# Kernel optimization log

Measured on AMD Instinct MI355X. Metric: run time of the kernel, lower is better.

## Reference

```python
import jax, jax.numpy as jnp
import numpy as np

INT8_MAX = 127.0

def setup_inputs() -> dict:
    key = jax.random.key(0)
    k1, k2, k3, k4 = jax.random.split(key, 4)
    B, T, IN, OUT = 1, 8192, 4096, 12288
    input_tensor = jax.random.normal(k1, (B, T, IN), dtype=jnp.float32)
    # pre-quantized int8 weight, symmetric range [-127, 127]
    weight = jax.random.randint(k2, (OUT, IN), -127, 128, dtype=jnp.int8)
    # per-output-row weight scales (small positive)
    weight_scale = (jax.random.uniform(k3, (OUT, 1), dtype=jnp.float32) * 0.01 + 1e-4)
    bias = jax.random.normal(k4, (OUT,), dtype=jnp.float32)
    return {"input_tensor": input_tensor, "weight": weight,
            "weight_scale": weight_scale, "bias": bias}

def reference(input_tensor, weight, weight_scale, bias):
    # input_tensor: [1, T, IN] -> squeeze leading dim as in torch forward
    x = input_tensor[0]  # [T, IN]
    # per-token symmetric int8 quantization (scaled_int8_quant, symmetric=True)
    absmax = jnp.max(jnp.abs(x), axis=-1, keepdims=True)            # [T, 1]
    x_scale = jnp.maximum(absmax, 1e-8) / INT8_MAX                  # [T, 1]
    x_q = jnp.clip(jnp.round(x / x_scale), -INT8_MAX, INT8_MAX).astype(jnp.int8)
    # int8 GEMM with int32 accumulation: [T, IN] x [IN, OUT]
    acc = jax.lax.dot_general(x_q, weight.T,
                              (((1,), (0,)), ((), ())),
                              preferred_element_type=jnp.int32)     # [T, OUT]
    # fused dequant epilogue: per-token scale * per-channel scale + bias
    out = acc.astype(jnp.float32) * x_scale * weight_scale[:, 0][None, :] + bias[None, :]
    return out[None]  # [1, T, OUT]
```

## Files before the change

kernel.cpp:

```cpp
#include <hip/hip_runtime.h>
#include <stdint.h>

#define T_TOKENS 8192
#define K_IN 4096
#define N_OUT 12288

using int32x4 = __attribute__((ext_vector_type(4))) int;

__global__ void quant_rows(const float* __restrict__ x,
                           int8_t* __restrict__ xq,
                           float* __restrict__ xs) {
    const int t = blockIdx.x;
    const int tid = threadIdx.x;
    const float* row = x + (size_t)t * K_IN;
    float4 v[4];
    float am = 0.0f;
#pragma unroll
    for (int i = 0; i < 4; ++i) {
        v[i] = ((const float4*)row)[tid + 256 * i];
        am = fmaxf(am, fmaxf(fmaxf(fabsf(v[i].x), fabsf(v[i].y)),
                             fmaxf(fabsf(v[i].z), fabsf(v[i].w))));
    }
#pragma unroll
    for (int off = 32; off > 0; off >>= 1)
        am = fmaxf(am, __shfl_xor(am, off));
    __shared__ float red[4];
    if ((tid & 63) == 0) red[tid >> 6] = am;
    __syncthreads();
    am = fmaxf(fmaxf(red[0], red[1]), fmaxf(red[2], red[3]));
    const float scale = fmaxf(am, 1e-8f) / 127.0f;
    if (tid == 0) xs[t] = scale;
    char4* dst = (char4*)(xq + (size_t)t * K_IN);
#pragma unroll
    for (int i = 0; i < 4; ++i) {
        float4 f = v[i];
        char4 c;
        float r;
        r = fminf(fmaxf(rintf(f.x / scale), -127.0f), 127.0f); c.x = (signed char)(int)r;
        r = fminf(fmaxf(rintf(f.y / scale), -127.0f), 127.0f); c.y = (signed char)(int)r;
        r = fminf(fmaxf(rintf(f.z / scale), -127.0f), 127.0f); c.z = (signed char)(int)r;
        r = fminf(fmaxf(rintf(f.w / scale), -127.0f), 127.0f); c.w = (signed char)(int)r;
        dst[tid + 256 * i] = c;
    }
}

__global__ void pack_weight(const int* __restrict__ w, int8_t* __restrict__ wq) {
    const int idx = blockIdx.x * 256 + threadIdx.x;
    int4 v = ((const int4*)w)[idx];
    char4 c;
    c.x = (signed char)v.x; c.y = (signed char)v.y;
    c.z = (signed char)v.z; c.w = (signed char)v.w;
    ((char4*)wq)[idx] = c;
}

__global__ __launch_bounds__(256) void gemm_i8(
        const int8_t* __restrict__ Aq, const int8_t* __restrict__ Bq,
        const float* __restrict__ xs, const float* __restrict__ wsc,
        const float* __restrict__ bias, float* __restrict__ out) {
    __shared__ __align__(16) int8_t smA[128 * 64];
    __shared__ __align__(16) int8_t smB[128 * 64];
    const int tid  = threadIdx.x;
    const int lane = tid & 63;
    const int w    = tid >> 6;
    const int m0   = blockIdx.y * 128;
    const int n0   = blockIdx.x * 128;
    const int wm   = (w >> 1) * 64;
    const int wn   = (w & 1) * 64;
    const int fr   = lane & 15;
    const int q    = lane >> 4;

    int32x4 acc[4][4] = {};

    int flati[2], rowi[2], kbsi[2];
#pragma unroll
    for (int i = 0; i < 2; ++i) {
        const int flat = i * 4096 + w * 1024 + lane * 16;
        const int row  = flat >> 6;
        const int kb   = (flat >> 4) & 3;
        flati[i] = flat;
        rowi[i]  = row;
        kbsi[i]  = (kb ^ ((row >> 1) & 3)) * 16;
    }

    for (int k0 = 0; k0 < K_IN; k0 += 64) {
#pragma unroll
        for (int i = 0; i < 2; ++i) {
            const int8_t* ga = Aq + (size_t)(m0 + rowi[i]) * K_IN + k0 + kbsi[i];
            const int8_t* gb = Bq + (size_t)(n0 + rowi[i]) * K_IN + k0 + kbsi[i];
            __builtin_amdgcn_global_load_lds(
                (const __attribute__((address_space(1))) void*)ga,
                (__attribute__((address_space(3))) void*)(&smA[flati[i]]), 16, 0, 0);
            __builtin_amdgcn_global_load_lds(
                (const __attribute__((address_space(1))) void*)gb,
                (__attribute__((address_space(3))) void*)(&smB[flati[i]]), 16, 0, 0);
        }
        __syncthreads();

        int32x4 af[4], bf[4];
#pragma unroll
        for (int im = 0; im < 4; ++im) {
            const int r  = wm + im * 16 + fr;
            const int kb = q ^ ((r >> 1) & 3);
            af[im] = *(const int32x4*)&smA[r * 64 + kb * 16];
        }
#pragma unroll
        for (int in = 0; in < 4; ++in) {
            const int r  = wn + in * 16 + fr;
            const int kb = q ^ ((r >> 1) & 3);
            bf[in] = *(const int32x4*)&smB[r * 64 + kb * 16];
        }
#pragma unroll
        for (int im = 0; im < 4; ++im)
#pragma unroll
            for (int in = 0; in < 4; ++in)
                acc[im][in] = __builtin_amdgcn_mfma_i32_16x16x64_i8(
                    af[im], bf[in], acc[im][in], 0, 0, 0);
        __syncthreads();
    }

#pragma unroll
    for (int im = 0; im < 4; ++im) {
#pragma unroll
        for (int i = 0; i < 4; ++i) {
            const int m = m0 + wm + im * 16 + q * 4 + i;
            const float sa = xs[m];
            float* orow = out + (size_t)m * N_OUT + n0;
#pragma unroll
            for (int in = 0; in < 4; ++in) {
                const int n = wn + in * 16 + fr;
                orow[n] = (float)acc[im][in][i] * sa * wsc[n0 + n] + bias[n0 + n];
            }
        }
    }
}

extern "C" void kernel_launch(void* const* d_in, const int* in_sizes, int n_in,
                              void* d_out, int out_size, void* d_ws, size_t ws_size,
                              hipStream_t stream) {
    const float* x    = (const float*)d_in[0];
    const int*   wgt  = (const int*)d_in[1];
    const float* wsc  = (const float*)d_in[2];
    const float* bias = (const float*)d_in[3];
    float* out = (float*)d_out;

    uint8_t* ws = (uint8_t*)d_ws;
    float*  xs = (float*)ws;
    int8_t* xq = (int8_t*)(ws + 32768);
    int8_t* wq = (int8_t*)(ws + 32768 + (size_t)T_TOKENS * K_IN);

    hipLaunchKernelGGL(pack_weight,
                       dim3(((size_t)N_OUT * K_IN) / 4 / 256), dim3(256), 0, stream,
                       wgt, wq);
    hipLaunchKernelGGL(quant_rows, dim3(T_TOKENS), dim3(256), 0, stream, x, xq, xs);
    hipLaunchKernelGGL(gemm_i8, dim3(N_OUT / 128, T_TOKENS / 128), dim3(256), 0, stream,
                       xq, wq, xs, wsc, bias, out);
}
```

Baseline: 1.117 ms.

## Rewrite int8 GEMM with 256x256x128 tiles, double-buffered LDS and ping-pong scheduling

Measured after the change: 934.9 us. 16.3% less time.

```diff
diff --git a/kernel.cpp b/kernel.cpp
--- a/kernel.cpp
+++ b/kernel.cpp
@@ -5,7 +5,17 @@
 #define K_IN 4096
 #define N_OUT 12288
 
+#define BM 256
+#define BN 256
+#define BK 128
+#define NT (K_IN / BK)
+#define GRID_X ((T_TOKENS / BM) * (N_OUT / BN))
+#define CPX (GRID_X / 8)
+
 using int32x4 = __attribute__((ext_vector_type(4))) int;
+
+#define BAR() do { asm volatile("" ::: "memory"); __builtin_amdgcn_s_barrier(); } while (0)
+#define LGKM0() asm volatile("s_waitcnt lgkmcnt(0)" ::: "memory")
 
 __global__ void quant_rows(const float* __restrict__ x,
                            int8_t* __restrict__ xq,
@@ -53,83 +63,160 @@
     ((char4*)wq)[idx] = c;
 }
 
-__global__ __launch_bounds__(256) void gemm_i8(
+template<int AR, int IL>
+__device__ __forceinline__ void mfma_quad(int32x4 (&acc)[8][4],
+                                          int32x4 (&a)[4][2],
+                                          int32x4 (&b)[4][2]) {
+#pragma unroll
+    for (int im = 0; im < 4; ++im)
+#pragma unroll
+        for (int in = 0; in < 2; ++in)
+#pragma unroll
+            for (int kk = 0; kk < 2; ++kk)
+                acc[AR + im][IL + in] = __builtin_amdgcn_mfma_i32_16x16x64_i8(
+                    a[im][kk], b[IL + in][kk], acc[AR + im][IL + in], 0, 0, 0);
+}
+
+__global__ __launch_bounds__(512, 2) void gemm_i8(
         const int8_t* __restrict__ Aq, const int8_t* __restrict__ Bq,
         const float* __restrict__ xs, const float* __restrict__ wsc,
         const float* __restrict__ bias, float* __restrict__ out) {
-    __shared__ __align__(16) int8_t smA[128 * 64];
-    __shared__ __align__(16) int8_t smB[128 * 64];
+    extern __shared__ int8_t sm[];
+
     const int tid  = threadIdx.x;
     const int lane = tid & 63;
-    const int w    = tid >> 6;
-    const int m0   = blockIdx.y * 128;
-    const int n0   = blockIdx.x * 128;
-    const int wm   = (w >> 1) * 64;
-    const int wn   = (w & 1) * 64;
+    const int wid  = tid >> 6;
+    const int wm   = wid >> 2;
+    const int wn   = wid & 3;
     const int fr   = lane & 15;
     const int q    = lane >> 4;
 
-    int32x4 acc[4][4] = {};
-
-    int flati[2], rowi[2], kbsi[2];
-#pragma unroll
-    for (int i = 0; i < 2; ++i) {
-        const int flat = i * 4096 + w * 1024 + lane * 16;
-        const int row  = flat >> 6;
-        const int kb   = (flat >> 4) & 3;
-        flati[i] = flat;
-        rowi[i]  = row;
-        kbsi[i]  = (kb ^ ((row >> 1) & 3)) * 16;
-    }
-
-    for (int k0 = 0; k0 < K_IN; k0 += 64) {
-#pragma unroll
-        for (int i = 0; i < 2; ++i) {
-            const int8_t* ga = Aq + (size_t)(m0 + rowi[i]) * K_IN + k0 + kbsi[i];
-            const int8_t* gb = Bq + (size_t)(n0 + rowi[i]) * K_IN + k0 + kbsi[i];
-            __builtin_amdgcn_global_load_lds(
-                (const __attribute__((address_space(1))) void*)ga,
-                (__attribute__((address_space(3))) void*)(&smA[flati[i]]), 16, 0, 0);
-            __builtin_amdgcn_global_load_lds(
-                (const __attribute__((address_space(1))) void*)gb,
-                (__attribute__((address_space(3))) void*)(&smB[flati[i]]), 16, 0, 0);
-        }
-        __syncthreads();
-
-        int32x4 af[4], bf[4];
+    const int bid = blockIdx.x;
+    const int swz = (bid & 7) * CPX + (bid >> 3);
+    const int tn  = swz % (N_OUT / BN);
+    const int tm  = swz / (N_OUT / BN);
+    const int m0  = tm * BM;
+    const int n0  = tn * BN;
+
+    const int f0   = tid * 16;
+    const int r0   = tid >> 3;
+    const int swzK = (((tid & 7) ^ ((tid >> 3) & 7)) << 4);
+    const int8_t* gA = Aq + (size_t)(m0 + r0) * K_IN + swzK;
+    const int8_t* gB = Bq + (size_t)(n0 + r0) * K_IN + swzK;
+
+    auto stageA = [&](int t, int half, int dbuf) {
+        const int8_t* src = gA + (size_t)half * (128 * K_IN) + t * BK;
+        int8_t* dst = sm + dbuf * 32768 + half * 16384 + f0;
+        __builtin_amdgcn_global_load_lds(
+            (const __attribute__((address_space(1))) void*)src,
+            (__attribute__((address_space(3))) void*)dst, 16, 0, 0);
+        __builtin_amdgcn_global_load_lds(
+            (const __attribute__((address_space(1))) void*)(src + (size_t)64 * K_IN),
+            (__attribute__((address_space(3))) void*)(dst + 8192), 16, 0, 0);
+    };
+    auto stageB = [&](int t, int half, int dbuf) {
+        const int8_t* src = gB + (size_t)half * (128 * K_IN) + t * BK;
+        int8_t* dst = sm + 65536 + dbuf * 32768 + half * 16384 + f0;
+        __builtin_amdgcn_global_load_lds(
+            (const __attribute__((address_space(1))) void*)src,
+            (__attribute__((address_space(3))) void*)dst, 16, 0, 0);
+        __builtin_amdgcn_global_load_lds(
+            (const __attribute__((address_space(1))) void*)(src + (size_t)64 * K_IN),
+            (__attribute__((address_space(3))) void*)(dst + 8192), 16, 0, 0);
+    };
+
+    const int aOff = wm * 16384 + fr * 128;
+    const int bOff = wn * 8192  + fr * 128;
+    const int kb0  = ((0 + q) ^ (fr & 7)) << 4;
+    const int kb1  = ((4 + q) ^ (fr & 7)) << 4;
+
+    int32x4 acc[8][4] = {};
+
+    stageB(0, 0, 0); stageA(0, 0, 0); stageB(0, 1, 0); stageA(0, 1, 0);
+    stageB(1, 0, 1); stageA(1, 0, 1);
+    asm volatile("s_waitcnt vmcnt(4)" ::: "memory");
+    BAR();
+
+    for (int j = 0; j < NT; ++j) {
+        const int buf = j & 1;
+        const int8_t* As = sm + buf * 32768;
+        const int8_t* Bs = sm + 65536 + buf * 32768;
+        int32x4 a[4][2], b[4][2];
+
 #pragma unroll
         for (int im = 0; im < 4; ++im) {
-            const int r  = wm + im * 16 + fr;
-            const int kb = q ^ ((r >> 1) & 3);
-            af[im] = *(const int32x4*)&smA[r * 64 + kb * 16];
-        }
-#pragma unroll
-        for (int in = 0; in < 4; ++in) {
-            const int r  = wn + in * 16 + fr;
-            const int kb = q ^ ((r >> 1) & 3);
-            bf[in] = *(const int32x4*)&smB[r * 64 + kb * 16];
-        }
-#pragma unroll
-        for (int im = 0; im < 4; ++im)
+            a[im][0] = *(const int32x4*)(As + aOff + im * 2048 + kb0);
+            a[im][1] = *(const int32x4*)(As + aOff + im * 2048 + kb1);
+        }
+#pragma unroll
+        for (int in = 0; in < 2; ++in) {
+            b[in][0] = *(const int32x4*)(Bs + bOff + in * 2048 + kb0);
+            b[in][1] = *(const int32x4*)(Bs + bOff + in * 2048 + kb1);
+        }
+        if (j + 1 < NT) stageB(j + 1, 1, buf ^ 1);
+        asm volatile("s_waitcnt lgkmcnt(8)" ::: "memory");
+        BAR();
+        LGKM0();
+        __builtin_amdgcn_s_setprio(1);
+        mfma_quad<0, 0>(acc, a, b);
+        __builtin_amdgcn_s_setprio(0);
+        BAR();
+
+#pragma unroll
+        for (int in = 0; in < 2; ++in) {
+            b[2 + in][0] = *(const int32x4*)(Bs + bOff + (2 + in) * 2048 + kb0);
+            b[2 + in][1] = *(const int32x4*)(Bs + bOff + (2 + in) * 2048 + kb1);
+        }
+        if (j + 1 < NT) stageA(j + 1, 1, buf ^ 1);
+        BAR();
+        LGKM0();
+        __builtin_amdgcn_s_setprio(1);
+        mfma_quad<0, 2>(acc, a, b);
+        __builtin_amdgcn_s_setprio(0);
+        BAR();
+
+#pragma unroll
+        for (int im = 0; im < 4; ++im) {
+            a[im][0] = *(const int32x4*)(As + aOff + 8192 + im * 2048 + kb0);
+            a[im][1] = *(const int32x4*)(As + aOff + 8192 + im * 2048 + kb1);
+        }
+        if (j + 2 < NT) stageB(j + 2, 0, buf);
+        BAR();
+        LGKM0();
+        __builtin_amdgcn_s_setprio(1);
+        mfma_quad<4, 2>(acc, a, b);
+        __builtin_amdgcn_s_setprio(0);
+        BAR();
+
+        if (j + 2 < NT) stageA(j + 2, 0, buf);
+        BAR();
+        __builtin_amdgcn_s_setprio(1);
+        mfma_quad<4, 0>(acc, a, b);
+        __builtin_amdgcn_s_setprio(0);
+        if (j < NT - 2)
+            asm volatile("s_waitcnt vmcnt(4)" ::: "memory");
+        else if (j == NT - 2)
+            asm volatile("s_waitcnt vmcnt(0)" ::: "memory");
+        BAR();
+    }
+
+    float wv[4], bv[4];
+#pragma unroll
+    for (int in = 0; in < 4; ++in) {
+        const int n = n0 + wn * 64 + in * 16 + fr;
+        wv[in] = wsc[n];
+        bv[in] = bias[n];
+    }
+#pragma unroll
+    for (int im = 0; im < 8; ++im) {
+#pragma unroll
+        for (int i = 0; i < 4; ++i) {
+            const int m = m0 + wm * 128 + im * 16 + q * 4 + i;
+            const float sa = xs[m];
+            float* orow = out + (size_t)m * N_OUT + n0 + wn * 64;
 #pragma unroll
             for (int in = 0; in < 4; ++in)
-                acc[im][in] = __builtin_amdgcn_mfma_i32_16x16x64_i8(
-                    af[im], bf[in], acc[im][in], 0, 0, 0);
-        __syncthreads();
-    }
-
-#pragma unroll
-    for (int im = 0; im < 4; ++im) {
-#pragma unroll
-        for (int i = 0; i < 4; ++i) {
-            const int m = m0 + wm + im * 16 + q * 4 + i;
-            const float sa = xs[m];
-            float* orow = out + (size_t)m * N_OUT + n0;
-#pragma unroll
-            for (int in = 0; in < 4; ++in) {
-                const int n = wn + in * 16 + fr;
-                orow[n] = (float)acc[im][in][i] * sa * wsc[n0 + n] + bias[n0 + n];
-            }
+                orow[in * 16 + fr] = (float)acc[im][in][i] * sa * wv[in] + bv[in];
         }
     }
 }
@@ -148,10 +235,17 @@
     int8_t* xq = (int8_t*)(ws + 32768);
     int8_t* wq = (int8_t*)(ws + 32768 + (size_t)T_TOKENS * K_IN);
 
+    static bool inited = false;
+    if (!inited) {
+        hipFuncSetAttribute((const void*)gemm_i8,
+                            hipFuncAttributeMaxDynamicSharedMemorySize, 131072);
+        inited = true;
+    }
+
     hipLaunchKernelGGL(pack_weight,
                        dim3(((size_t)N_OUT * K_IN) / 4 / 256), dim3(256), 0, stream,
                        wgt, wq);
     hipLaunchKernelGGL(quant_rows, dim3(T_TOKENS), dim3(256), 0, stream, x, xq, xs);
-    hipLaunchKernelGGL(gemm_i8, dim3(N_OUT / 128, T_TOKENS / 128), dim3(256), 0, stream,
+    hipLaunchKernelGGL(gemm_i8, dim3(GRID_X), dim3(512), 131072, stream,
                        xq, wq, xs, wsc, bias, out);
 }
```
